# Kernel tuning notes

Hardware: AMD Instinct MI355X
Metric: run time of the kernel (lower is better)

## Reference

```python
import jax, jax.numpy as jnp
import numpy as np


def _lstm(x, h0, c0, Wih, Whh, b):
    """Single-layer LSTM, batch_first input x: [B,T,D]. PyTorch gate order i,f,g,o.
    Returns (h_seq [T,B,H], h_T [B,H], c_T [B,H])."""
    xs = jnp.swapaxes(x, 0, 1)  # [T,B,D]

    def step(carry, xt):
        h, c = carry
        gates = xt @ Wih.T + h @ Whh.T + b  # [B,4H]
        i, f, g, o = jnp.split(gates, 4, axis=-1)
        c = jax.nn.sigmoid(f) * c + jax.nn.sigmoid(i) * jnp.tanh(g)
        h = jax.nn.sigmoid(o) * jnp.tanh(c)
        return (h, c), h

    (h, c), hs = jax.lax.scan(step, (h0, c0), xs)
    return hs, h, c


def setup_inputs() -> dict:
    key = jax.random.key(0)
    ks = jax.random.split(key, 16)
    B, T, Tf, Tu = 256, 365, 15, 76
    Dh, Df, Du, H = 64, 32, 16, 256
    s = 1.0 / np.sqrt(H)  # torch-style uniform scale, approximated with scaled normals
    return {
        "x_d": jax.random.normal(ks[0], (B, T, Dh), jnp.float32),
        "x_f": jax.random.normal(ks[1], (B, Tf, Df), jnp.float32),
        "x_ff": jax.random.normal(ks[2], (B, Tu, Du), jnp.float32),
        "enc_Wih": jax.random.normal(ks[3], (4 * H, Dh), jnp.float32) * s,
        "enc_Whh": jax.random.normal(ks[4], (4 * H, H), jnp.float32) * s,
        "enc_b": jax.random.normal(ks[5], (4 * H,), jnp.float32) * s,
        "decf_Wih": jax.random.normal(ks[6], (4 * H, Df), jnp.float32) * s,
        "decf_Whh": jax.random.normal(ks[7], (4 * H, H), jnp.float32) * s,
        "decf_b": jax.random.normal(ks[8], (4 * H,), jnp.float32) * s,
        "decu_Wih": jax.random.normal(ks[9], (4 * H, Du), jnp.float32) * s,
        "decu_Whh": jax.random.normal(ks[10], (4 * H, H), jnp.float32) * s,
        "decu_b": jax.random.normal(ks[11], (4 * H,), jnp.float32) * s,
        "head_W": jax.random.normal(ks[12], (1, H), jnp.float32) * s,
        "head_b": jax.random.normal(ks[13], (1,), jnp.float32) * s,
    }


def reference(x_d, x_f, x_ff, enc_Wih, enc_Whh, enc_b,
              decf_Wih, decf_Whh, decf_b, decu_Wih, decu_Whh, decu_b,
              head_W, head_b):
    B = x_d.shape[0]
    H = enc_Whh.shape[1]
    Tf = x_f.shape[1]
    Tu = x_ff.shape[1]
    horizon = Tf + Tu
    h0 = jnp.zeros((B, H), x_d.dtype)
    c0 = jnp.zeros((B, H), x_d.dtype)

    # Encoder over historical sequence
    _, h, c = _lstm(x_d, h0, c0, enc_Wih, enc_Whh, enc_b)

    # Forecast decoder: one LSTM step per horizon step + linear head (dropout = eval identity)
    hs_f, h, c = _lstm(x_f, h, c, decf_Wih, decf_Whh, decf_b)  # [Tf,B,H]
    out_f = (jnp.einsum('tbh,oh->tbo', hs_f, head_W)[..., 0] + head_b[0]).T  # [B,Tf]

    # Future decoder, continuing the hidden state
    hs_u, h, c = _lstm(x_ff, h, c, decu_Wih, decu_Whh, decu_b)  # [Tu,B,H]
    out_u = (jnp.einsum('tbh,oh->tbo', hs_u, head_W)[..., 0] + head_b[0]).T  # [B,Tu]

    # Faithful to original: both loops write outputs[:, t], so the future loop
    # overwrites the first Tu columns.
    outputs = jnp.zeros((B, horizon), x_d.dtype)
    outputs = outputs.at[:, :Tf].set(out_f)
    outputs = outputs.at[:, :Tu].set(out_u)
    return outputs
```

## Files before the change

### kernel.cpp

```cpp
#include <hip/hip_runtime.h>
#include <stdint.h>


typedef __attribute__((ext_vector_type(8))) short short8;
typedef __attribute__((ext_vector_type(4))) float f32x4;
typedef __attribute__((ext_vector_type(2))) unsigned int u32x2;

#define L2E 1.4426950408889634f

__device__ __forceinline__ uint16_t f2bf(float f) {
  uint32_t x = __float_as_uint(f);
  x += 0x7fffu + ((x >> 16) & 1u);
  return (uint16_t)(x >> 16);
}
__device__ __forceinline__ uint32_t pk2(float a, float b) {
  return (uint32_t)f2bf(a) | ((uint32_t)f2bf(b) << 16);
}
__device__ __forceinline__ uint32_t cvtpk(float lo, float hi) {
  uint32_t r;
  asm("v_cvt_pk_bf16_f32 %0, %1, %2" : "=v"(r) : "v"(lo), "v"(hi));
  return r;
}
__device__ __forceinline__ float bfhalf(uint32_t w, int hi) {
  return __uint_as_float(hi ? (w & 0xffff0000u) : (w << 16));
}
__device__ __forceinline__ f32x4 MFMA(short8 a, short8 b, f32x4 c) {
  return __builtin_amdgcn_mfma_f32_16x16x32_bf16(a, b, c, 0, 0, 0);
}
__device__ __forceinline__ float ex2(float x) { return __builtin_amdgcn_exp2f(x); }
__device__ __forceinline__ float rcp(float x) { return __builtin_amdgcn_rcpf(x); }

__device__ __forceinline__ void lgkm_barrier() {
  __builtin_amdgcn_sched_barrier(0);
  asm volatile("s_waitcnt lgkmcnt(0)" ::: "memory");
  __builtin_amdgcn_s_barrier();
  __builtin_amdgcn_sched_barrier(0);
}

__global__ void init_kernel(float* c_state, uint16_t* h_state, float* out) {
  int i = blockIdx.x * 256 + threadIdx.x;
  if (i < 65536) { c_state[i] = 0.f; h_state[i] = 0; }
  if (i < 256 * 91) out[i] = 0.f;
}

template <int DIN>
__global__ __launch_bounds__(512) void xproj_kernel(
    const float* __restrict__ x, const float* __restrict__ Wih,
    const float* __restrict__ bias, uint32_t* __restrict__ xp,
    int t0, int T) {
  const int tid = threadIdx.x, w = tid >> 6, l = tid & 63;
  const int l16 = l & 15, lg = l >> 4;
  const int tc = blockIdx.x >> 1;
  const int sub = blockIdx.x & 1;
  const int t = t0 + tc;
  constexpr int KT = (DIN + 31) / 32;

  short8 bfr[8][KT];
  float4 bias4[8];
#pragma unroll
  for (int ni = 0; ni < 8; ++ni) {
    const int n = (w * 8 + ni) * 16 + l16;
    bias4[ni] = *(const float4*)&bias[(w * 8 + ni) * 16 + lg * 4];
#pragma unroll
    for (int kt = 0; kt < KT; ++kt) {
      const int k0 = kt * 32 + lg * 8;
      short8 fr;
#pragma unroll
      for (int e = 0; e < 8; ++e) fr[e] = 0;
      if (k0 + 8 <= DIN) {
        const float* s = Wih + (size_t)n * DIN + k0;
#pragma unroll
        for (int e = 0; e < 8; ++e) fr[e] = (short)f2bf(s[e]);
      }
      bfr[ni][kt] = fr;
    }
  }

  for (int mi = 0; mi < 8; ++mi) {
    const int btile = sub * 8 + mi;
    const int b = btile * 16 + l16;
    short8 af[KT];
#pragma unroll
    for (int kt = 0; kt < KT; ++kt) {
      const int k0 = kt * 32 + lg * 8;
      short8 fr;
#pragma unroll
      for (int e = 0; e < 8; ++e) fr[e] = 0;
      if (k0 + 8 <= DIN) {
        const float* s = x + ((size_t)b * T + t) * DIN + k0;
#pragma unroll
        for (int e = 0; e < 8; ++e) fr[e] = (short)f2bf(s[e]);
      }
      af[kt] = fr;
    }
#pragma unroll
    for (int ni = 0; ni < 8; ++ni) {
      f32x4 acc = {0.f, 0.f, 0.f, 0.f};
#pragma unroll
      for (int kt = 0; kt < KT; ++kt) acc = MFMA(bfr[ni][kt], af[kt], acc);
      const int nt = w * 8 + ni;
      size_t idx = ((((size_t)tc * 16 + btile) * 64 + nt) * 64 + l) * 2;
      u32x2 v;
      v[0] = pk2(acc[0] + bias4[ni].x, acc[1] + bias4[ni].y);
      v[1] = pk2(acc[2] + bias4[ni].z, acc[3] + bias4[ni].w);
      *(u32x2*)(xp + idx) = v;
    }
  }
}

template <int DO_HEAD>
__global__ __launch_bounds__(512, 2) void rec_kernel(
    const uint32_t* __restrict__ xp, const float* __restrict__ Whh,
    float* __restrict__ c_state, uint16_t* __restrict__ h_state,
    float* __restrict__ out, const float* __restrict__ headW,
    const float* __restrict__ headb, int ct, int tcol0) {
  __shared__ short8 B_lds[8 * 16 * 64];
  __shared__ uint16_t h_lds[2][16][264];
  __shared__ float headbuf[2][16][8];

  const int tid = threadIdx.x, w = tid >> 6, l = tid & 63;
  const int l16 = l & 15, lg = l >> 4;
  const int blk = blockIdx.x, b0 = blk * 16;

  short8 bv[48];
#pragma unroll
  for (int g = 0; g < 4; ++g)
#pragma unroll
    for (int nt = 0; nt < 2; ++nt)
#pragma unroll
      for (int kt = 0; kt < 8; ++kt) {
        const int row = (g * 16 + w * 2 + nt) * 16 + l16;
        const float* s = Whh + (size_t)row * 256 + kt * 32 + lg * 8;
        short8 fr;
#pragma unroll
        for (int e = 0; e < 8; ++e) fr[e] = (short)f2bf(s[e]);
        const int tile = g * 2 + nt;
        if (kt <= 5) bv[tile * 6 + kt] = fr;
        else B_lds[(w * 16 + (kt - 6) * 8 + tile) * 64 + l] = fr;
      }

  float c_reg[2][4];
#pragma unroll
  for (int nt = 0; nt < 2; ++nt) {
    float4 c4 = *(const float4*)&c_state[(size_t)(b0 + l16) * 256 +
                                         (w * 2 + nt) * 16 + lg * 4];
    c_reg[nt][0] = c4.x; c_reg[nt][1] = c4.y;
    c_reg[nt][2] = c4.z; c_reg[nt][3] = c4.w;
  }
  for (int idx = tid; idx < 16 * 256; idx += 512)
    h_lds[0][idx >> 8][idx & 255] = h_state[(size_t)(b0 + (idx >> 8)) * 256 + (idx & 255)];
  float4 hw4[2];
#pragma unroll
  for (int nt = 0; nt < 2; ++nt)
    hw4[nt] = *(const float4*)&headW[(w * 2 + nt) * 16 + lg * 4];
  const float hb = headb[0];

  const uint32_t* xpb = xp + ((size_t)(blk * 64 + w * 2) * 64 + l) * 2;
  u32x2 xpf[2][4];
#pragma unroll
  for (int nt = 0; nt < 2; ++nt)
#pragma unroll
    for (int g = 0; g < 4; ++g)
      xpf[nt][g] = *(const u32x2*)(xpb + (size_t)g * 2048 + nt * 128);

  __syncthreads();

  for (int t = 0; t < ct; ++t) {
    const int cur = t & 1, nxt = cur ^ 1;
    const int tn = (t + 1 < ct) ? t + 1 : t;
    float hp = 0.f;

#pragma unroll
    for (int nt = 0; nt < 2; ++nt) {
      f32x4 acc[4];
      {
        short8 hf = *(const short8*)(&h_lds[cur][l16][lg * 8]);
#pragma unroll
        for (int g = 0; g < 4; ++g)
          acc[g] = MFMA(bv[(g * 2 + nt) * 6], hf, f32x4{0.f, 0.f, 0.f, 0.f});
      }
#pragma unroll
      for (int kt = 1; kt <= 5; ++kt) {
        short8 hf = *(const short8*)(&h_lds[cur][l16][kt * 32 + lg * 8]);
#pragma unroll
        for (int g = 0; g < 4; ++g)
          acc[g] = MFMA(bv[(g * 2 + nt) * 6 + kt], hf, acc[g]);
      }
#pragma unroll
      for (int kt = 6; kt <= 7; ++kt) {
        short8 hf = *(const short8*)(&h_lds[cur][l16][kt * 32 + lg * 8]);
#pragma unroll
        for (int g = 0; g < 4; ++g)
          acc[g] = MFMA(B_lds[(w * 16 + (kt - 6) * 8 + g * 2 + nt) * 64 + l], hf, acc[g]);
      }

      float hv[4];
#pragma unroll
      for (int j = 0; j < 4; ++j) {
        const int hi = j & 1, wd = j >> 1;
        float gi = acc[0][j] + bfhalf(xpf[nt][0][wd], hi);
        float gf = acc[1][j] + bfhalf(xpf[nt][1][wd], hi);
        float gg = acc[2][j] + bfhalf(xpf[nt][2][wd], hi);
        float go = acc[3][j] + bfhalf(xpf[nt][3][wd], hi);
        float ei = ex2(-gi * L2E);
        float eg = ex2(fminf(2.f * gg * L2E, 80.f));
        float sitg = (eg - 1.f) * rcp((1.f + ei) * (eg + 1.f));
        float ef = ex2(-gf * L2E);
        float cc = fmaf(c_reg[nt][j], rcp(1.f + ef), sitg);
        c_reg[nt][j] = cc;
        float eo = ex2(-go * L2E);
        float ec = ex2(fminf(2.f * cc * L2E, 80.f));
        float hh = (ec - 1.f) * rcp((1.f + eo) * (ec + 1.f));
        hv[j] = hh;
      }
      if (DO_HEAD) {
        hp = fmaf(hv[0], hw4[nt].x, hp); hp = fmaf(hv[1], hw4[nt].y, hp);
        hp = fmaf(hv[2], hw4[nt].z, hp); hp = fmaf(hv[3], hw4[nt].w, hp);
      }
      {
        u32x2 hwrd;
        hwrd[0] = cvtpk(hv[0], hv[1]);
        hwrd[1] = cvtpk(hv[2], hv[3]);
        *(u32x2*)(&h_lds[nxt][l16][(w * 2 + nt) * 16 + lg * 4]) = hwrd;
      }
#pragma unroll
      for (int g = 0; g < 4; ++g)
        xpf[nt][g] = *(const u32x2*)(xpb + (size_t)tn * 131072 + g * 2048 + nt * 128);
    }

    if (DO_HEAD) {
      float s = hp;
      s += __shfl_xor(s, 16);
      s += __shfl_xor(s, 32);
      if (lg == 0) headbuf[t & 1][l16][w] = s;
    }

    lgkm_barrier();

    if (DO_HEAD) {
      if (tid < 16) {
        const float* hbp = headbuf[t & 1][tid];
        float s = hbp[0] + hbp[1] + hbp[2] + hbp[3] + hbp[4] + hbp[5] + hbp[6] + hbp[7];
        out[(size_t)(b0 + tid) * 91 + (tcol0 + t)] = s + hb;
      }
    }
  }

#pragma unroll
  for (int nt = 0; nt < 2; ++nt) {
    float4 c4 = {c_reg[nt][0], c_reg[nt][1], c_reg[nt][2], c_reg[nt][3]};
    *(float4*)&c_state[(size_t)(b0 + l16) * 256 + (w * 2 + nt) * 16 + lg * 4] = c4;
  }
  for (int idx = tid; idx < 16 * 256; idx += 512)
    h_state[(size_t)(b0 + (idx >> 8)) * 256 + (idx & 255)] = h_lds[ct & 1][idx >> 8][idx & 255];
}

extern "C" void kernel_launch(void* const* d_in, const int* in_sizes, int n_in,
                              void* d_out, int out_size, void* d_ws, size_t ws_size,
                              hipStream_t stream) {
  const float* headW = (const float*)d_in[12];
  const float* headb = (const float*)d_in[13];
  float* out = (float*)d_out;

  char* ws = (char*)d_ws;
  float* c_state = (float*)ws;
  uint16_t* h_state = (uint16_t*)(ws + 262144);
  uint32_t* xp = (uint32_t*)(ws + 393216);

  int ct_max = 1;
  if (ws_size > 393216 + 512 * 1024) {
    size_t c = (ws_size - 393216) / (512 * 1024);
    ct_max = (c > 365) ? 365 : (int)c;
  }

  init_kernel<<<256, 256, 0, stream>>>(c_state, h_state, out);

  struct Phase { const float* x; const float* Wih; const float* Whh; const float* b; int T; int D; int head; };
  Phase ph[3] = {
      {(const float*)d_in[0], (const float*)d_in[3], (const float*)d_in[4], (const float*)d_in[5],
       in_sizes[0] / (256 * 64), 64, 0},
      {(const float*)d_in[1], (const float*)d_in[6], (const float*)d_in[7], (const float*)d_in[8],
       in_sizes[1] / (256 * 32), 32, 0},
      {(const float*)d_in[2], (const float*)d_in[9], (const float*)d_in[10], (const float*)d_in[11],
       in_sizes[2] / (256 * 16), 16, 1},
  };

  for (int pi = 0; pi < 3; ++pi) {
    const Phase& P = ph[pi];
    for (int t0 = 0; t0 < P.T; t0 += ct_max) {
      int ct = (P.T - t0 < ct_max) ? (P.T - t0) : ct_max;
      dim3 g(ct * 2);
      if (P.D == 64)
        xproj_kernel<64><<<g, 512, 0, stream>>>(P.x, P.Wih, P.b, xp, t0, P.T);
      else if (P.D == 32)
        xproj_kernel<32><<<g, 512, 0, stream>>>(P.x, P.Wih, P.b, xp, t0, P.T);
      else
        xproj_kernel<16><<<g, 512, 0, stream>>>(P.x, P.Wih, P.b, xp, t0, P.T);
      if (P.head)
        rec_kernel<1><<<16, 512, 0, stream>>>(xp, P.Whh, c_state, h_state, out,
                                              headW, headb, ct, t0);
      else
        rec_kernel<0><<<16, 512, 0, stream>>>(xp, P.Whh, c_state, h_state, out,
                                              headW, headb, ct, t0);
    }
  }
}
```

Measured before the change: 1.382 ms.

## XOR-swizzle h LDS layout, hoist h fragment loads, prescale gate preactivations

The padded h_lds row stride is replaced by an unpadded layout with an XOR swizzle keyed on the batch row, and reads, writes and state copies are remapped to match. All eight h fragments are loaded from LDS up front, once per step instead of once per nt pass, so both passes reuse them. The input projection now stores gate preactivations already multiplied by -log2(e) or 2*log2(e), which folds the scale into one fma in the recurrent loop. The hoisted fragments add register pressure in a kernel that already keeps 48 weight fragments in VGPRs.

Measured after the change: 1.837 ms. 1.33x slower.

```diff
diff --git a/kernel.cpp b/kernel.cpp
--- a/kernel.cpp
+++ b/kernel.cpp
@@ -99,10 +99,11 @@
 #pragma unroll
       for (int kt = 0; kt < KT; ++kt) acc = MFMA(bfr[ni][kt], af[kt], acc);
       const int nt = w * 8 + ni;
+      const float sc = ((nt >> 4) == 2) ? (2.f * L2E) : -L2E;
       size_t idx = ((((size_t)tc * 16 + btile) * 64 + nt) * 64 + l) * 2;
       u32x2 v;
-      v[0] = pk2(acc[0] + bias4[ni].x, acc[1] + bias4[ni].y);
-      v[1] = pk2(acc[2] + bias4[ni].z, acc[3] + bias4[ni].w);
+      v[0] = pk2((acc[0] + bias4[ni].x) * sc, (acc[1] + bias4[ni].y) * sc);
+      v[1] = pk2((acc[2] + bias4[ni].z) * sc, (acc[3] + bias4[ni].w) * sc);
       *(u32x2*)(xp + idx) = v;
     }
   }
@@ -115,12 +116,13 @@
     float* __restrict__ out, const float* __restrict__ headW,
     const float* __restrict__ headb, int ct, int tcol0) {
   __shared__ short8 B_lds[8 * 16 * 64];
-  __shared__ uint16_t h_lds[2][16][264];
+  __shared__ uint16_t h_lds[2][16][256];
   __shared__ float headbuf[2][16][8];
 
   const int tid = threadIdx.x, w = tid >> 6, l = tid & 63;
   const int l16 = l & 15, lg = l >> 4;
   const int blk = blockIdx.x, b0 = blk * 16;
+  const int swz = (l16 & 7) << 3;
 
   short8 bv[48];
 #pragma unroll
@@ -147,8 +149,10 @@
     c_reg[nt][0] = c4.x; c_reg[nt][1] = c4.y;
     c_reg[nt][2] = c4.z; c_reg[nt][3] = c4.w;
   }
-  for (int idx = tid; idx < 16 * 256; idx += 512)
-    h_lds[0][idx >> 8][idx & 255] = h_state[(size_t)(b0 + (idx >> 8)) * 256 + (idx & 255)];
+  for (int idx = tid; idx < 16 * 256; idx += 512) {
+    const int b = idx >> 8, c = idx & 255;
+    h_lds[0][b][c ^ ((b & 7) << 3)] = h_state[(size_t)(b0 + b) * 256 + c];
+  }
   float4 hw4[2];
 #pragma unroll
   for (int nt = 0; nt < 2; ++nt)
@@ -170,45 +174,39 @@
     const int tn = (t + 1 < ct) ? t + 1 : t;
     float hp = 0.f;
 
+    short8 hf[8];
+#pragma unroll
+    for (int kt = 0; kt < 8; ++kt)
+      hf[kt] = *(const short8*)(&h_lds[cur][l16][(kt * 32 + lg * 8) ^ swz]);
+
 #pragma unroll
     for (int nt = 0; nt < 2; ++nt) {
       f32x4 acc[4];
-      {
-        short8 hf = *(const short8*)(&h_lds[cur][l16][lg * 8]);
+#pragma unroll
+      for (int g = 0; g < 4; ++g)
+        acc[g] = MFMA(bv[(g * 2 + nt) * 6], hf[0], f32x4{0.f, 0.f, 0.f, 0.f});
+#pragma unroll
+      for (int kt = 1; kt <= 5; ++kt)
 #pragma unroll
         for (int g = 0; g < 4; ++g)
-          acc[g] = MFMA(bv[(g * 2 + nt) * 6], hf, f32x4{0.f, 0.f, 0.f, 0.f});
-      }
-#pragma unroll
-      for (int kt = 1; kt <= 5; ++kt) {
-        short8 hf = *(const short8*)(&h_lds[cur][l16][kt * 32 + lg * 8]);
+          acc[g] = MFMA(bv[(g * 2 + nt) * 6 + kt], hf[kt], acc[g]);
+#pragma unroll
+      for (int kt = 6; kt <= 7; ++kt)
 #pragma unroll
         for (int g = 0; g < 4; ++g)
-          acc[g] = MFMA(bv[(g * 2 + nt) * 6 + kt], hf, acc[g]);
-      }
-#pragma unroll
-      for (int kt = 6; kt <= 7; ++kt) {
-        short8 hf = *(const short8*)(&h_lds[cur][l16][kt * 32 + lg * 8]);
-#pragma unroll
-        for (int g = 0; g < 4; ++g)
-          acc[g] = MFMA(B_lds[(w * 16 + (kt - 6) * 8 + g * 2 + nt) * 64 + l], hf, acc[g]);
-      }
+          acc[g] = MFMA(B_lds[(w * 16 + (kt - 6) * 8 + g * 2 + nt) * 64 + l], hf[kt], acc[g]);
 
       float hv[4];
 #pragma unroll
       for (int j = 0; j < 4; ++j) {
         const int hi = j & 1, wd = j >> 1;
-        float gi = acc[0][j] + bfhalf(xpf[nt][0][wd], hi);
-        float gf = acc[1][j] + bfhalf(xpf[nt][1][wd], hi);
-        float gg = acc[2][j] + bfhalf(xpf[nt][2][wd], hi);
-        float go = acc[3][j] + bfhalf(xpf[nt][3][wd], hi);
-        float ei = ex2(-gi * L2E);
-        float eg = ex2(fminf(2.f * gg * L2E, 80.f));
+        float ei = ex2(fmaf(acc[0][j], -L2E, bfhalf(xpf[nt][0][wd], hi)));
+        float eg = ex2(fminf(fmaf(acc[2][j], 2.f * L2E, bfhalf(xpf[nt][2][wd], hi)), 80.f));
         float sitg = (eg - 1.f) * rcp((1.f + ei) * (eg + 1.f));
-        float ef = ex2(-gf * L2E);
+        float ef = ex2(fmaf(acc[1][j], -L2E, bfhalf(xpf[nt][1][wd], hi)));
         float cc = fmaf(c_reg[nt][j], rcp(1.f + ef), sitg);
         c_reg[nt][j] = cc;
-        float eo = ex2(-go * L2E);
+        float eo = ex2(fmaf(acc[3][j], -L2E, bfhalf(xpf[nt][3][wd], hi)));
         float ec = ex2(fminf(2.f * cc * L2E, 80.f));
         float hh = (ec - 1.f) * rcp((1.f + eo) * (ec + 1.f));
         hv[j] = hh;
@@ -221,7 +219,7 @@
         u32x2 hwrd;
         hwrd[0] = cvtpk(hv[0], hv[1]);
         hwrd[1] = cvtpk(hv[2], hv[3]);
-        *(u32x2*)(&h_lds[nxt][l16][(w * 2 + nt) * 16 + lg * 4]) = hwrd;
+        *(u32x2*)(&h_lds[nxt][l16][((w * 2 + nt) * 16 + lg * 4) ^ swz]) = hwrd;
       }
 #pragma unroll
       for (int g = 0; g < 4; ++g)
@@ -251,8 +249,10 @@
     float4 c4 = {c_reg[nt][0], c_reg[nt][1], c_reg[nt][2], c_reg[nt][3]};
     *(float4*)&c_state[(size_t)(b0 + l16) * 256 + (w * 2 + nt) * 16 + lg * 4] = c4;
   }
-  for (int idx = tid; idx < 16 * 256; idx += 512)
-    h_state[(size_t)(b0 + (idx >> 8)) * 256 + (idx & 255)] = h_lds[ct & 1][idx >> 8][idx & 255];
+  for (int idx = tid; idx < 16 * 256; idx += 512) {
+    const int b = idx >> 8, c = idx & 255;
+    h_state[(size_t)(b0 + b) * 256 + c] = h_lds[ct & 1][b][c ^ ((b & 7) << 3)];
+  }
 }
 
 extern "C" void kernel_launch(void* const* d_in, const int* in_sizes, int n_in,
```
